# Optimization experiments

Hardware: AMD Instinct MI355X
Metric: run time of the kernel (lower is better)

Reference implementation:

```python
import jax, jax.numpy as jnp
import numpy as np

N, D = 8192, 256
TEMPERATURE = 1.0
K_NEIGHBORS = 5  # min(5, N-1)
EPS = 1e-08


def setup_inputs() -> dict:
    key = jax.random.key(0)
    k1, k2 = jax.random.split(key)
    node_embeddings = jax.random.normal(k1, (N, D), dtype=jnp.float32)
    adj_matrix = jax.random.uniform(k2, (N, N), dtype=jnp.float32)
    return {"node_embeddings": node_embeddings, "adj_matrix": adj_matrix}


def _components(node_embeddings, adj_matrix):
    n = node_embeddings.shape[0]

    # --- total energy ---
    kinetic = jnp.sum(node_embeddings ** 2, axis=-1)  # [N]
    neighbor_emb = adj_matrix @ node_embeddings       # [N, D]
    potential = -jnp.sum(node_embeddings * neighbor_emb, axis=-1)
    degrees = jnp.sum(adj_matrix, axis=-1)
    total_energy = kinetic + potential / (degrees + EPS)

    # --- local entropy (cosine sims masked by adjacency, softmax rowwise) ---
    norms = jnp.linalg.norm(node_embeddings, axis=-1, keepdims=True)
    normalized = node_embeddings / jnp.maximum(norms, 1e-12)  # F.normalize eps
    similarities = normalized @ normalized.T                  # [N, N]
    masked = similarities * adj_matrix
    row_sums = jnp.sum(adj_matrix, axis=1)
    probs = jax.nn.softmax(masked / TEMPERATURE, axis=1)
    ent = -jnp.sum(probs * jnp.log(probs + EPS), axis=1)
    local_entropy = jnp.where(row_sums > 0, ent, 0.0)

    # --- equilibrium deviation (global + KNN-local) ---
    global_mean = jnp.mean(node_embeddings, axis=0, keepdims=True)
    global_dev = jnp.linalg.norm(node_embeddings - global_mean, axis=-1)
    sq = jnp.sum(node_embeddings ** 2, axis=-1)
    d2 = sq[:, None] + sq[None, :] - 2.0 * (node_embeddings @ node_embeddings.T)
    dist = jnp.sqrt(jnp.maximum(d2, 0.0))  # torch.cdist equivalent
    _, topk_idx = jax.lax.top_k(-dist, K_NEIGHBORS + 1)  # smallest k+1
    neighbor_idx = topk_idx[:, 1:]                        # drop self, [N, K]
    local_means = jnp.mean(node_embeddings[neighbor_idx], axis=1)  # [N, D]
    local_dev = jnp.linalg.norm(node_embeddings - local_means, axis=-1)
    equilibrium_deviation = 0.6 * global_dev + 0.4 * local_dev

    # --- structural centrality ---
    degree_centrality = degrees / (n - 1 + EPS)
    emb_norms = jnp.linalg.norm(node_embeddings, axis=-1)
    emb_centrality = emb_norms / (jnp.max(emb_norms) + EPS)
    structural_centrality = 0.5 * degree_centrality + 0.5 * emb_centrality

    return jnp.stack([total_energy, local_entropy, equilibrium_deviation, structural_centrality])  # [4, N]


def reference(node_embeddings, adj_matrix):
    return _components(node_embeddings, adj_matrix)
```

## Files before the change

### kernel.cpp

```cpp
#include <hip/hip_runtime.h>
#include <math.h>

#define N 8192
#define D 256
#define EPSF 1e-8f
#define NJS 2
#define ROWS 32
#define JSPAN 4096
#define NCH 32
#define NU 128

#define WS_SQ    0
#define WS_RINV  (N)
#define WS_GMEAN (2*N)
#define WS_MAXN  (2*N+256)
#define WS_COLP  (2*N+512)
#define WS_P0    (2*N+512+65536)
#define WS_EBF   (WS_P0+56*N)

typedef __attribute__((ext_vector_type(8))) short bf16x8;
typedef __attribute__((ext_vector_type(4))) float f32x4;

__device__ __forceinline__ unsigned short f2bf(float f) {
    unsigned u = __float_as_uint(f);
    u += 0x7fffu + ((u >> 16) & 1u);
    return (unsigned short)(u >> 16);
}

#if __has_builtin(__builtin_amdgcn_fmed3f)
#define MED3(a,b,c) __builtin_amdgcn_fmed3f((a),(b),(c))
#else
#define MED3(a,b,c) fmaxf(fminf((a),(b)), fminf(fmaxf((a),(b)),(c)))
#endif

#define PINS(T, x) do {                                                         \
    float _x = (x);                                                             \
    float _n0 = fminf((T)[0], _x);                                              \
    float _n1 = MED3((T)[0], (T)[1], _x);                                       \
    float _n2 = MED3((T)[1], (T)[2], _x);                                       \
    float _n3 = MED3((T)[2], (T)[3], _x);                                       \
    float _n4 = MED3((T)[3], (T)[4], _x);                                       \
    (T)[0]=_n0; (T)[1]=_n1; (T)[2]=_n2; (T)[3]=_n3; (T)[4]=_n4;                 \
  } while (0)

__global__ void k_prep(const float* __restrict__ emb, float* __restrict__ ws,
                       unsigned short* __restrict__ ebf) {
    if (blockIdx.x < 2048) {
        int row = blockIdx.x * 4 + (threadIdx.x >> 6);
        int lane = threadIdx.x & 63;
        float4 v = *(const float4*)(emb + (size_t)row * D + lane * 4);
        ushort4 b;
        b.x = f2bf(v.x); b.y = f2bf(v.y); b.z = f2bf(v.z); b.w = f2bf(v.w);
        *(ushort4*)(ebf + (size_t)row * D + lane * 4) = b;
        float s = v.x * v.x + v.y * v.y + v.z * v.z + v.w * v.w;
#pragma unroll
        for (int mk = 32; mk >= 1; mk >>= 1) s += __shfl_xor(s, mk);
        if (lane == 0) {
            ws[WS_SQ + row] = s;
            ws[WS_RINV + row] = 1.0f / fmaxf(sqrtf(s), 1e-12f);
        }
    } else {
        int d = threadIdx.x;
        int b = blockIdx.x - 2048;
        float s = 0.f;
        for (int r = b * 32; r < b * 32 + 32; ++r) s += emb[(size_t)r * D + d];
        ws[WS_COLP + b * 256 + d] = s;
    }
}

__global__ void k_colred(float* __restrict__ ws) {
    __shared__ float red[256];
    int d = threadIdx.x;
    float s = 0.f;
    for (int b = 0; b < 256; ++b) s += ws[WS_COLP + b * 256 + d];
    ws[WS_GMEAN + d] = s * (1.0f / N);
    float mx = 0.f;
    for (int i = d; i < N; i += 256) mx = fmaxf(mx, ws[WS_SQ + i]);
    red[d] = mx;
    __syncthreads();
#pragma unroll
    for (int st2 = 128; st2 >= 1; st2 >>= 1) {
        if (d < st2) red[d] = fmaxf(red[d], red[d + st2]);
        __syncthreads();
    }
    if (d == 0) ws[WS_MAXN] = sqrtf(red[0]);
}

#define STAGE(PTR, U) do {                                                      \
    const int _u = (U);                                                         \
    const int _cc2 = _u >> 2, _k0 = (_u & 3) << 6;                              \
    const size_t _rb = (size_t)(j0 + _cc2 * 128 + (w << 5) + srow) * D + _k0 + (sc << 3); \
    _Pragma("unroll")                                                           \
    for (int q = 0; q < 4; ++q) {                                               \
      __builtin_amdgcn_global_load_lds(                                         \
        (const __attribute__((address_space(1))) void*)(ebf + _rb + (size_t)(q << 3) * D), \
        (__attribute__((address_space(3))) void*)&(PTR)[((w << 5) + (q << 3)) * 64], \
        16, 0, 0);                                                              \
    } } while (0)

#define VMW(NLIT) do {                                                          \
    asm volatile("s_waitcnt vmcnt(" #NLIT ")" ::: "memory");                    \
    __builtin_amdgcn_sched_barrier(0);                                          \
  } while (0)

#define SBAR() __builtin_amdgcn_sched_barrier(0)

#define COMP(PTR, H) do {                                                       \
    _Pragma("unroll")                                                           \
    for (int ksl = 0; ksl < 2; ++ksl) {                                         \
      const int pg = ((ksl << 2) + g) ^ (lid & 7);                              \
      bf16x8 afr[2];                                                            \
      _Pragma("unroll")                                                         \
      for (int mf = 0; mf < 2; ++mf)                                            \
        afr[mf] = *(const bf16x8*)&(PTR)[((w << 5) + (mf << 4) + lid) * 64 + (pg << 3)]; \
      _Pragma("unroll")                                                         \
      for (int nf = 0; nf < 2; ++nf)                                            \
        _Pragma("unroll")                                                       \
        for (int mf = 0; mf < 2; ++mf)                                          \
          acc[nf][mf] = __builtin_amdgcn_mfma_f32_16x16x32_bf16(                \
              afr[mf], bfr[nf][(H) * 2 + ksl], acc[nf][mf], 0, 0, 0);           \
    } } while (0)

__global__ __launch_bounds__(256) void k_main(
    const float* __restrict__ adj,
    const unsigned short* __restrict__ ebf,
    const float* __restrict__ ws,
    float* __restrict__ pout)
{
    __shared__ unsigned short tile[3][128 * 64];

    const int tid = threadIdx.x;
    const int w = tid >> 6;
    const int l = tid & 63;
    const int lid = l & 15;
    const int g = l >> 4;
    const int srow = l >> 3;
    const int sc = (l & 7) ^ srow;
    const int panel = blockIdx.x >> 1;
    const int js = blockIdx.x & 1;
    const int row0 = panel * ROWS;
    const int j0 = js * JSPAN;

    const float* sq = ws + WS_SQ;
    const float* rinv = ws + WS_RINV;

    bf16x8 bfr[2][8];
    float rvr[2];
    int r_[2];
#pragma unroll
    for (int nf = 0; nf < 2; ++nf) {
        int r = row0 + nf * 16 + lid;
        r_[nf] = r;
        rvr[nf] = rinv[r];
#pragma unroll
        for (int ks = 0; ks < 8; ++ks)
            bfr[nf][ks] = *(const bf16x8*)(ebf + (size_t)r * D + ks * 32 + g * 8);
    }

    float deg[2] = {0.f, 0.f}, pot[2] = {0.f, 0.f};
    float sl[2] = {0.f, 0.f}, st[2] = {0.f, 0.f};
    float tv[2][5];
#pragma unroll
    for (int nf = 0; nf < 2; ++nf)
#pragma unroll
        for (int s2 = 0; s2 < 5; ++s2) tv[nf][s2] = 1e30f;

    f32x4 acc[2][2];
#pragma unroll
    for (int nf = 0; nf < 2; ++nf)
#pragma unroll
        for (int mf = 0; mf < 2; ++mf) acc[nf][mf] = (f32x4){0.f, 0.f, 0.f, 0.f};
    f32x4 advA[2][2], sqv[2], rvv[2];

    unsigned short* p0 = &tile[0][0];
    unsigned short* p1 = &tile[1][0];
    unsigned short* p2 = &tile[2][0];

    STAGE(p0, 0);
    STAGE(p1, 1);

#pragma unroll 1
    for (int cc = 0; cc < NCH; ++cc) {
        const int u0 = cc << 2;
        const int jj = j0 + cc * 128 + (w << 5);

        STAGE(p2, (u0 + 2) & (NU - 1));
#pragma unroll
        for (int nf = 0; nf < 2; ++nf)
#pragma unroll
            for (int mf = 0; mf < 2; ++mf)
                advA[nf][mf] = __builtin_nontemporal_load(
                    (const f32x4*)(adj + (size_t)r_[nf] * N + jj + mf * 16 + g * 4));
        VMW(12);
        COMP(p0, 0);

#pragma unroll
        for (int mf = 0; mf < 2; ++mf) {
            sqv[mf] = *(const f32x4*)(sq + jj + mf * 16 + g * 4);
            rvv[mf] = *(const f32x4*)(rinv + jj + mf * 16 + g * 4);
        }
        SBAR();
        STAGE(p0, (u0 + 3) & (NU - 1));
        VMW(16);
        COMP(p1, 1);

        SBAR();
        STAGE(p1, (u0 + 4) & (NU - 1));
        VMW(16);
        COMP(p2, 2);

        SBAR();
        STAGE(p2, (u0 + 5) & (NU - 1));
        VMW(8);
        COMP(p0, 3);
#pragma unroll
        for (int nf = 0; nf < 2; ++nf) {
#pragma unroll
            for (int mf = 0; mf < 2; ++mf) {
#pragma unroll
                for (int e = 0; e < 4; ++e) {
                    const float gv = acc[nf][mf][e];
                    const float a = advA[nf][mf][e];
                    const int j = jj + mf * 16 + g * 4 + e;
                    deg[nf] += a;
                    pot[nf] = fmaf(a, gv, pot[nf]);
                    const float s = (gv * rvr[nf]) * (rvv[mf][e] * a);
                    const float ex = __expf(s);
                    sl[nf] += ex;
                    st[nf] = fmaf(ex, s, st[nf]);
                    float dp = fmaf(-2.f, gv, sqv[mf][e]);
                    dp = (j == r_[nf]) ? 1e30f : dp;
                    const float key = __uint_as_float(
                        (__float_as_uint(dp) & 0xFFFFE000u) | (unsigned)j);
                    PINS(tv[nf], key);
                }
                acc[nf][mf] = (f32x4){0.f, 0.f, 0.f, 0.f};
            }
        }

        unsigned short* tmp = p0; p0 = p1; p1 = p2; p2 = tmp;
    }

#pragma unroll
    for (int nf = 0; nf < 2; ++nf) {
#pragma unroll
        for (int mk = 16; mk <= 32; mk <<= 1) {
            deg[nf] += __shfl_xor(deg[nf], mk);
            pot[nf] += __shfl_xor(pot[nf], mk);
            sl[nf] += __shfl_xor(sl[nf], mk);
            st[nf] += __shfl_xor(st[nf], mk);
            float ok[5];
#pragma unroll
            for (int s2 = 0; s2 < 5; ++s2) ok[s2] = __shfl_xor(tv[nf][s2], mk);
#pragma unroll
            for (int s2 = 0; s2 < 5; ++s2) PINS(tv[nf], ok[s2]);
        }
    }

    __syncthreads();
    float* lds_s = (float*)&tile[0][0];
    float* lds_k = lds_s + 4 * 32 * 4;
#pragma unroll
    for (int nf = 0; nf < 2; ++nf) {
        if (g == 0) {
            int lr = nf * 16 + lid;
            lds_s[(w * 32 + lr) * 4 + 0] = deg[nf];
            lds_s[(w * 32 + lr) * 4 + 1] = pot[nf];
            lds_s[(w * 32 + lr) * 4 + 2] = sl[nf];
            lds_s[(w * 32 + lr) * 4 + 3] = st[nf];
#pragma unroll
            for (int s2 = 0; s2 < 5; ++s2)
                lds_k[(w * 32 + lr) * 5 + s2] = tv[nf][s2];
        }
    }
    __syncthreads();

    if (tid < 32) {
        float dg = 0.f, pt = 0.f, ll = 0.f, tt = 0.f;
#pragma unroll
        for (int w2 = 0; w2 < 4; ++w2) {
            dg += lds_s[(w2 * 32 + tid) * 4 + 0];
            pt += lds_s[(w2 * 32 + tid) * 4 + 1];
            ll += lds_s[(w2 * 32 + tid) * 4 + 2];
            tt += lds_s[(w2 * 32 + tid) * 4 + 3];
        }
        float mk5[5];
#pragma unroll
        for (int s2 = 0; s2 < 5; ++s2) mk5[s2] = lds_k[tid * 5 + s2];
#pragma unroll
        for (int w2 = 1; w2 < 4; ++w2)
#pragma unroll
            for (int s2 = 0; s2 < 5; ++s2)
                PINS(mk5, lds_k[(w2 * 32 + tid) * 5 + s2]);
        const int slot = js * N + row0 + tid;
        pout[slot] = dg;
        pout[2 * N + slot] = pt;
        pout[4 * N + slot] = ll;
        pout[6 * N + slot] = tt;
#pragma unroll
        for (int s2 = 0; s2 < 5; ++s2)
            pout[8 * N + slot * 5 + s2] = mk5[s2];
    }
}

__global__ void k_final(const float* __restrict__ emb, const float* __restrict__ ws,
                        float* __restrict__ out) {
    int row = blockIdx.x * 4 + (threadIdx.x >> 6);
    int lane = threadIdx.x & 63;
    const float* p0 = ws + WS_P0;

    float dg = 0.f, pt = 0.f, ll = 0.f, tt = 0.f;
#pragma unroll
    for (int js = 0; js < NJS; ++js) {
        int slot = js * N + row;
        dg += p0[slot]; pt += p0[2 * N + slot];
        ll += p0[4 * N + slot]; tt += p0[6 * N + slot];
    }

    float keys[5];
#pragma unroll
    for (int s = 0; s < 5; ++s) keys[s] = p0[8 * N + (size_t)row * 5 + s];
#pragma unroll
    for (int s = 0; s < 5; ++s) PINS(keys, p0[8 * N + (size_t)(N + row) * 5 + s]);
    int nb[5];
#pragma unroll
    for (int t = 0; t < 5; ++t) nb[t] = (int)(__float_as_uint(keys[t]) & 0x1FFFu);

    float4 e = *(const float4*)(emb + (size_t)row * D + lane * 4);
    float4 gm = *(const float4*)(ws + WS_GMEAN + lane * 4);
    float gx = e.x - gm.x, gy = e.y - gm.y, gz = e.z - gm.z, gw = e.w - gm.w;
    float gd = gx * gx + gy * gy + gz * gz + gw * gw;
    float ax = 0.f, ay = 0.f, az = 0.f, aw = 0.f;
#pragma unroll
    for (int t = 0; t < 5; ++t) {
        float4 nv = *(const float4*)(emb + (size_t)nb[t] * D + lane * 4);
        ax += nv.x; ay += nv.y; az += nv.z; aw += nv.w;
    }
    ax *= 0.2f; ay *= 0.2f; az *= 0.2f; aw *= 0.2f;
    float lx = e.x - ax, ly = e.y - ay, lz = e.z - az, lw = e.w - aw;
    float ld = lx * lx + ly * ly + lz * lz + lw * lw;
#pragma unroll
    for (int mk = 32; mk >= 1; mk >>= 1) {
        gd += __shfl_xor(gd, mk);
        ld += __shfl_xor(ld, mk);
    }
    if (lane == 0) {
        float sqv = ws[WS_SQ + row];
        float mn = ws[WS_MAXN];
        float ent = logf(ll) - tt / ll;
        out[row] = sqv - pt / (dg + EPSF);
        out[N + row] = (dg > 0.f) ? ent : 0.f;
        out[2 * N + row] = 0.6f * sqrtf(gd) + 0.4f * sqrtf(ld);
        out[3 * N + row] = 0.5f * (dg / (8191.0f + EPSF)) + 0.5f * (sqrtf(sqv) / (mn + EPSF));
    }
}

extern "C" void kernel_launch(void* const* d_in, const int* in_sizes, int n_in,
                              void* d_out, int out_size, void* d_ws, size_t ws_size,
                              hipStream_t stream) {
    const float* emb = (const float*)d_in[0];
    const float* adj = (const float*)d_in[1];
    float* out = (float*)d_out;
    float* ws = (float*)d_ws;
    unsigned short* ebf = (unsigned short*)(ws + WS_EBF);

    k_prep<<<2304, 256, 0, stream>>>(emb, ws, ebf);
    k_colred<<<1, 256, 0, stream>>>(ws);
    k_main<<<512, 256, 0, stream>>>(adj, ebf, ws, ws + WS_P0);
    k_final<<<N / 4, 256, 0, stream>>>(emb, ws, out);
}
```

Baseline: 157.2 us.

## Use four fixed LDS stages per chunk and track top-6 instead of masking self

```diff
diff --git a/kernel.cpp b/kernel.cpp
--- a/kernel.cpp
+++ b/kernel.cpp
@@ -8,7 +8,6 @@
 #define ROWS 32
 #define JSPAN 4096
 #define NCH 32
-#define NU 128
 
 #define WS_SQ    0
 #define WS_RINV  (N)
@@ -33,14 +32,15 @@
 #define MED3(a,b,c) fmaxf(fminf((a),(b)), fminf(fmaxf((a),(b)),(c)))
 #endif
 
-#define PINS(T, x) do {                                                         \
+#define PINS6(T, x) do {                                                        \
     float _x = (x);                                                             \
     float _n0 = fminf((T)[0], _x);                                              \
     float _n1 = MED3((T)[0], (T)[1], _x);                                       \
     float _n2 = MED3((T)[1], (T)[2], _x);                                       \
     float _n3 = MED3((T)[2], (T)[3], _x);                                       \
     float _n4 = MED3((T)[3], (T)[4], _x);                                       \
-    (T)[0]=_n0; (T)[1]=_n1; (T)[2]=_n2; (T)[3]=_n3; (T)[4]=_n4;                 \
+    float _n5 = MED3((T)[4], (T)[5], _x);                                       \
+    (T)[0]=_n0; (T)[1]=_n1; (T)[2]=_n2; (T)[3]=_n3; (T)[4]=_n4; (T)[5]=_n5;     \
   } while (0)
 
 __global__ void k_prep(const float* __restrict__ emb, float* __restrict__ ws,
@@ -86,14 +86,11 @@
     if (d == 0) ws[WS_MAXN] = sqrtf(red[0]);
 }
 
-#define STAGE(PTR, U) do {                                                      \
-    const int _u = (U);                                                         \
-    const int _cc2 = _u >> 2, _k0 = (_u & 3) << 6;                              \
-    const size_t _rb = (size_t)(j0 + _cc2 * 128 + (w << 5) + srow) * D + _k0 + (sc << 3); \
+#define STAGE(PTR, SOFF, K0) do {                                               \
     _Pragma("unroll")                                                           \
     for (int q = 0; q < 4; ++q) {                                               \
       __builtin_amdgcn_global_load_lds(                                         \
-        (const __attribute__((address_space(1))) void*)(ebf + _rb + (size_t)(q << 3) * D), \
+        (const __attribute__((address_space(1))) void*)(ebf + gbase + (SOFF) + (K0) + q * (8 * D)), \
         (__attribute__((address_space(3))) void*)&(PTR)[((w << 5) + (q << 3)) * 64], \
         16, 0, 0);                                                              \
     } } while (0)
@@ -127,7 +124,10 @@
     const float* __restrict__ ws,
     float* __restrict__ pout)
 {
-    __shared__ unsigned short tile[3][128 * 64];
+    __shared__ unsigned short tile0[128 * 64];
+    __shared__ unsigned short tile1[128 * 64];
+    __shared__ unsigned short tile2[128 * 64];
+    __shared__ unsigned short tile3[128 * 64];
 
     const int tid = threadIdx.x;
     const int w = tid >> 6;
@@ -143,6 +143,7 @@
 
     const float* sq = ws + WS_SQ;
     const float* rinv = ws + WS_RINV;
+    const size_t gbase = (size_t)(j0 + (w << 5) + srow) * D + (sc << 3);
 
     bf16x8 bfr[2][8];
     float rvr[2];
@@ -159,11 +160,11 @@
 
     float deg[2] = {0.f, 0.f}, pot[2] = {0.f, 0.f};
     float sl[2] = {0.f, 0.f}, st[2] = {0.f, 0.f};
-    float tv[2][5];
+    float tv[2][6];
 #pragma unroll
     for (int nf = 0; nf < 2; ++nf)
 #pragma unroll
-        for (int s2 = 0; s2 < 5; ++s2) tv[nf][s2] = 1e30f;
+        for (int s2 = 0; s2 < 6; ++s2) tv[nf][s2] = 1e30f;
 
     f32x4 acc[2][2];
 #pragma unroll
@@ -172,47 +173,46 @@
         for (int mf = 0; mf < 2; ++mf) acc[nf][mf] = (f32x4){0.f, 0.f, 0.f, 0.f};
     f32x4 advA[2][2], sqv[2], rvv[2];
 
-    unsigned short* p0 = &tile[0][0];
-    unsigned short* p1 = &tile[1][0];
-    unsigned short* p2 = &tile[2][0];
-
-    STAGE(p0, 0);
-    STAGE(p1, 1);
+    STAGE(tile0, 0, 0);
+    STAGE(tile1, 0, 64);
+    STAGE(tile2, 0, 128);
+    STAGE(tile3, 0, 192);
 
 #pragma unroll 1
     for (int cc = 0; cc < NCH; ++cc) {
-        const int u0 = cc << 2;
         const int jj = j0 + cc * 128 + (w << 5);
-
-        STAGE(p2, (u0 + 2) & (NU - 1));
+        const size_t snext = (size_t)(cc + 1) * (128 * D);
+
 #pragma unroll
         for (int nf = 0; nf < 2; ++nf)
 #pragma unroll
             for (int mf = 0; mf < 2; ++mf)
                 advA[nf][mf] = __builtin_nontemporal_load(
                     (const f32x4*)(adj + (size_t)r_[nf] * N + jj + mf * 16 + g * 4));
-        VMW(12);
-        COMP(p0, 0);
+        VMW(16);
+        COMP(tile0, 0);
+        SBAR();
+        STAGE(tile0, snext, 0);
 
 #pragma unroll
         for (int mf = 0; mf < 2; ++mf) {
             sqv[mf] = *(const f32x4*)(sq + jj + mf * 16 + g * 4);
             rvv[mf] = *(const f32x4*)(rinv + jj + mf * 16 + g * 4);
         }
+        VMW(20);
+        COMP(tile1, 1);
         SBAR();
-        STAGE(p0, (u0 + 3) & (NU - 1));
+        STAGE(tile1, snext, 64);
+
         VMW(16);
-        COMP(p1, 1);
-
+        COMP(tile2, 2);
         SBAR();
-        STAGE(p1, (u0 + 4) & (NU - 1));
-        VMW(16);
-        COMP(p2, 2);
-
+        STAGE(tile2, snext, 128);
+
+        VMW(8);
+        COMP(tile3, 3);
         SBAR();
-        STAGE(p2, (u0 + 5) & (NU - 1));
-        VMW(8);
-        COMP(p0, 3);
+        STAGE(tile3, snext, 192);
 #pragma unroll
         for (int nf = 0; nf < 2; ++nf) {
 #pragma unroll
@@ -228,17 +228,14 @@
                     const float ex = __expf(s);
                     sl[nf] += ex;
                     st[nf] = fmaf(ex, s, st[nf]);
-                    float dp = fmaf(-2.f, gv, sqv[mf][e]);
-                    dp = (j == r_[nf]) ? 1e30f : dp;
+                    const float dp = fmaf(-2.f, gv, sqv[mf][e]);
                     const float key = __uint_as_float(
                         (__float_as_uint(dp) & 0xFFFFE000u) | (unsigned)j);
-                    PINS(tv[nf], key);
+                    PINS6(tv[nf], key);
                 }
                 acc[nf][mf] = (f32x4){0.f, 0.f, 0.f, 0.f};
             }
         }
-
-        unsigned short* tmp = p0; p0 = p1; p1 = p2; p2 = tmp;
     }
 
 #pragma unroll
@@ -249,16 +246,16 @@
             pot[nf] += __shfl_xor(pot[nf], mk);
             sl[nf] += __shfl_xor(sl[nf], mk);
             st[nf] += __shfl_xor(st[nf], mk);
-            float ok[5];
-#pragma unroll
-            for (int s2 = 0; s2 < 5; ++s2) ok[s2] = __shfl_xor(tv[nf][s2], mk);
-#pragma unroll
-            for (int s2 = 0; s2 < 5; ++s2) PINS(tv[nf], ok[s2]);
+            float ok[6];
+#pragma unroll
+            for (int s2 = 0; s2 < 6; ++s2) ok[s2] = __shfl_xor(tv[nf][s2], mk);
+#pragma unroll
+            for (int s2 = 0; s2 < 6; ++s2) PINS6(tv[nf], ok[s2]);
         }
     }
 
     __syncthreads();
-    float* lds_s = (float*)&tile[0][0];
+    float* lds_s = (float*)&tile0[0];
     float* lds_k = lds_s + 4 * 32 * 4;
 #pragma unroll
     for (int nf = 0; nf < 2; ++nf) {
@@ -269,8 +266,8 @@
             lds_s[(w * 32 + lr) * 4 + 2] = sl[nf];
             lds_s[(w * 32 + lr) * 4 + 3] = st[nf];
 #pragma unroll
-            for (int s2 = 0; s2 < 5; ++s2)
-                lds_k[(w * 32 + lr) * 5 + s2] = tv[nf][s2];
+            for (int s2 = 0; s2 < 6; ++s2)
+                lds_k[(w * 32 + lr) * 6 + s2] = tv[nf][s2];
         }
     }
     __syncthreads();
@@ -284,22 +281,22 @@
             ll += lds_s[(w2 * 32 + tid) * 4 + 2];
             tt += lds_s[(w2 * 32 + tid) * 4 + 3];
         }
-        float mk5[5];
-#pragma unroll
-        for (int s2 = 0; s2 < 5; ++s2) mk5[s2] = lds_k[tid * 5 + s2];
+        float mk6[6];
+#pragma unroll
+        for (int s2 = 0; s2 < 6; ++s2) mk6[s2] = lds_k[tid * 6 + s2];
 #pragma unroll
         for (int w2 = 1; w2 < 4; ++w2)
 #pragma unroll
-            for (int s2 = 0; s2 < 5; ++s2)
-                PINS(mk5, lds_k[(w2 * 32 + tid) * 5 + s2]);
+            for (int s2 = 0; s2 < 6; ++s2)
+                PINS6(mk6, lds_k[(w2 * 32 + tid) * 6 + s2]);
         const int slot = js * N + row0 + tid;
         pout[slot] = dg;
         pout[2 * N + slot] = pt;
         pout[4 * N + slot] = ll;
         pout[6 * N + slot] = tt;
 #pragma unroll
-        for (int s2 = 0; s2 < 5; ++s2)
-            pout[8 * N + slot * 5 + s2] = mk5[s2];
+        for (int s2 = 0; s2 < 6; ++s2)
+            pout[8 * N + slot * 6 + s2] = mk6[s2];
     }
 }
 
@@ -317,14 +314,14 @@
         ll += p0[4 * N + slot]; tt += p0[6 * N + slot];
     }
 
-    float keys[5];
-#pragma unroll
-    for (int s = 0; s < 5; ++s) keys[s] = p0[8 * N + (size_t)row * 5 + s];
-#pragma unroll
-    for (int s = 0; s < 5; ++s) PINS(keys, p0[8 * N + (size_t)(N + row) * 5 + s]);
+    float keys[6];
+#pragma unroll
+    for (int s = 0; s < 6; ++s) keys[s] = p0[8 * N + (size_t)row * 6 + s];
+#pragma unroll
+    for (int s = 0; s < 6; ++s) PINS6(keys, p0[8 * N + (size_t)(N + row) * 6 + s]);
     int nb[5];
 #pragma unroll
-    for (int t = 0; t < 5; ++t) nb[t] = (int)(__float_as_uint(keys[t]) & 0x1FFFu);
+    for (int t = 0; t < 5; ++t) nb[t] = (int)(__float_as_uint(keys[t + 1]) & 0x1FFFu);
 
     float4 e = *(const float4*)(emb + (size_t)row * D + lane * 4);
     float4 gm = *(const float4*)(ws + WS_GMEAN + lane * 4);
```

After: 159.5 us. Within noise of the previous version (+1.5%).
